# Optimization experiments

Measured on AMD Instinct MI355X. Metric: run time of the kernel, lower is better.

Reference implementation:

```python
import jax, jax.numpy as jnp
import numpy as np

N_NODES = 100000

def gcn_conv(x, W, b, src, dst, n):
    # PyG GCNConv with add_self_loops=True, symmetric normalization.
    # Transform first (reduces feature dim before irregular aggregation).
    h = x @ W  # [N, out]
    # degree with self loops: in-degree over dst plus 1 per node
    deg = jax.ops.segment_sum(jnp.ones_like(dst, dtype=h.dtype), dst, num_segments=n) + 1.0
    dinv = jax.lax.rsqrt(deg)  # deg >= 1 due to self loops
    norm = dinv[src] * dinv[dst]  # [E]
    # message = norm * h[src], aggregated at dst; self-loop term = dinv_i^2 * h_i
    agg = jax.ops.segment_sum(h[src] * norm[:, None], dst, num_segments=n)
    agg = agg + h * (dinv * dinv)[:, None]
    return agg + b

def setup_inputs() -> dict:
    key = jax.random.key(0)
    k1, k2, k3, k4, k5 = jax.random.split(key, 5)
    F_in, H, E_dim = 128, 64, 64
    node_features = jax.random.normal(k1, (N_NODES, F_in), dtype=jnp.float32)
    edge_index = jax.random.randint(k2, (2, 1600000), 0, N_NODES, dtype=jnp.int64)
    s = 1.0 / np.sqrt(F_in)
    W1 = jax.random.uniform(k3, (F_in, H), jnp.float32, -s, s)
    b1 = jnp.zeros((H,), jnp.float32)
    s2 = 1.0 / np.sqrt(H)
    W2 = jax.random.uniform(k4, (H, H), jnp.float32, -s2, s2)
    b2 = jnp.zeros((H,), jnp.float32)
    Wl = jax.random.uniform(k5, (H, E_dim), jnp.float32, -s2, s2)
    bl = jnp.zeros((E_dim,), jnp.float32)
    return {"node_features": node_features, "edge_index": edge_index,
            "W1": W1, "b1": b1, "W2": W2, "b2": b2, "Wl": Wl, "bl": bl}

def reference(node_features, edge_index, W1, b1, W2, b2, Wl, bl):
    src, dst = edge_index[0], edge_index[1]
    n = node_features.shape[0]
    x = node_features.astype(jnp.float32)
    x = jax.nn.relu(gcn_conv(x, W1, b1, src, dst, n))
    # dropout: train=False -> identity
    x = jax.nn.relu(gcn_conv(x, W2, b2, src, dst, n))
    x = x @ Wl + bl
    return jax.nn.sigmoid(x).T  # [embed_size, N]
```

## Files before the change

### kernel.cpp

```cpp
#include <hip/hip_runtime.h>
#include <hip/hip_bf16.h>


#define FEAT 64
#define FIN 128
#define PAD 64
#define CAP 4608
#define EPB 2048
#define MAXNB 512

typedef __attribute__((ext_vector_type(8))) short  short8;
typedef __attribute__((ext_vector_type(4))) float  f32x4;
typedef __attribute__((ext_vector_type(2))) float  float2v;

__device__ __forceinline__ unsigned short f2bf(float f) {
    union { float f; unsigned u; } x; x.f = f;
    unsigned r = x.u + 0x7FFF + ((x.u >> 16) & 1);
    return (unsigned short)(r >> 16);
}
__device__ __forceinline__ float bflo(unsigned u) {
    union { unsigned v; float f; } x; x.v = u << 16; return x.f;
}
__device__ __forceinline__ float bfhi(unsigned u) {
    union { unsigned v; float f; } x; x.v = u & 0xFFFF0000u; return x.f;
}

__global__ void wtrans_kernel(const float* __restrict__ W1, const float* __restrict__ W2,
                              const float* __restrict__ Wl,
                              unsigned short* __restrict__ Wt1, unsigned short* __restrict__ Wt2,
                              unsigned short* __restrict__ Wlt, int* __restrict__ bcnt) {
    int t = blockIdx.x * 256 + threadIdx.x;
    if (t < FIN * 64) {
        int k = t >> 6, n = t & 63;
        Wt1[n * FIN + k] = f2bf(W1[t]);
    } else if (t < FIN * 64 + 64 * 64) {
        int u = t - FIN * 64;
        int k = u >> 6, n = u & 63;
        Wt2[n * 64 + k] = f2bf(W2[u]);
    } else if (t < FIN * 64 + 2 * 64 * 64) {
        int u = t - FIN * 64 - 64 * 64;
        int k = u >> 6, n = u & 63;
        Wlt[n * 64 + k] = f2bf(Wl[u]);
    } else if (t < FIN * 64 + 2 * 64 * 64 + MAXNB * 16) {
        bcnt[t - FIN * 64 - 2 * 64 * 64] = 0;
    }
}

__global__ __launch_bounds__(256) void bin_kernel(const int* __restrict__ ei,
                                                  int* __restrict__ bcnt,
                                                  int* __restrict__ bbuf,
                                                  int E, int nb) {
    __shared__ int hist[MAXNB];
    __shared__ int base[MAXNB];
    for (int t = threadIdx.x; t < nb; t += 256) hist[t] = 0;
    __syncthreads();
    int e0 = blockIdx.x * EPB;
    int sreg[8], dreg[8], preg[8];
#pragma unroll
    for (int k = 0; k < 8; ++k) {
        int idx = e0 + k * 256 + threadIdx.x;
        if (idx < E) {
            sreg[k] = ei[idx];
            dreg[k] = ei[E + idx];
            preg[k] = atomicAdd(&hist[dreg[k] >> 8], 1);
        } else {
            dreg[k] = -1;
        }
    }
    __syncthreads();
    for (int t = threadIdx.x; t < nb; t += 256) {
        int h = hist[t];
        base[t] = (h > 0) ? atomicAdd(&bcnt[t * 16], h) : 0;
    }
    __syncthreads();
#pragma unroll
    for (int k = 0; k < 8; ++k) {
        if (dreg[k] >= 0) {
            int b = dreg[k] >> 8;
            int p = base[b] + preg[k];
            if (p < CAP)
                bbuf[(size_t)b * CAP + p] = sreg[k] | ((dreg[k] & 255) << 20);
        }
    }
}

__global__ __launch_bounds__(256) void ell_from_bins_kernel(const int* __restrict__ bbuf,
                                                            const int* __restrict__ bcnt,
                                                            int* __restrict__ col,
                                                            int* __restrict__ cnt,
                                                            float* __restrict__ dinv,
                                                            unsigned int* __restrict__ gz,
                                                            int N) {
    __shared__ int lcnt[256];
    int b = blockIdx.x;
    int d0 = b << 8;
    lcnt[threadIdx.x] = 0;
    if (b == 0 && threadIdx.x < 32)
        gz[(size_t)N * 32 + threadIdx.x] = 0u;
    __syncthreads();
    int ne = bcnt[b * 16];
    if (ne > CAP) ne = CAP;
    const int* eb = bbuf + (size_t)b * CAP;
    for (int i = threadIdx.x; i < ne; i += 256) {
        int w = eb[i];
        int s = w & 0xFFFFF;
        int dl = w >> 20;
        int slot = atomicAdd(&lcnt[dl], 1);
        if (slot < PAD) col[(size_t)(d0 + dl) * PAD + slot] = s;
    }
    __syncthreads();
    int d = d0 + threadIdx.x;
    if (d < N) {
        int c = lcnt[threadIdx.x];
        if (c > PAD) c = PAD;
        int c8 = (c + 7) & ~7;
        for (int k = c; k < c8; ++k) col[(size_t)d * PAD + k] = N;
        cnt[d] = c;
        dinv[d] = rsqrtf((float)c + 1.0f);
    }
}

__global__ __launch_bounds__(256) void gemm1_mfma_kernel(const float* __restrict__ x,
                                                         const unsigned short* __restrict__ Wt,
                                                         const float* __restrict__ dinv,
                                                         unsigned short* __restrict__ g, int N) {
    const int lane = threadIdx.x & 63;
    const int wave = threadIdx.x >> 6;
    const int m = lane & 15, quad = lane >> 4;
    const int r0 = blockIdx.x * 64 + wave * 16;
    const int arow = r0 + m;
    const bool aok = arow < N;
    f32x4 acc[4] = {f32x4{0,0,0,0}, f32x4{0,0,0,0}, f32x4{0,0,0,0}, f32x4{0,0,0,0}};
    union { short8 s; unsigned short u[8]; } a;
#pragma unroll
    for (int s = 0; s < FIN / 32; ++s) {
        if (aok) {
            const float* xp = x + (size_t)arow * FIN + s * 32 + quad * 8;
            float4 a0 = *(const float4*)xp;
            float4 a1 = *(const float4*)(xp + 4);
            a.u[0] = f2bf(a0.x); a.u[1] = f2bf(a0.y);
            a.u[2] = f2bf(a0.z); a.u[3] = f2bf(a0.w);
            a.u[4] = f2bf(a1.x); a.u[5] = f2bf(a1.y);
            a.u[6] = f2bf(a1.z); a.u[7] = f2bf(a1.w);
        } else {
#pragma unroll
            for (int k = 0; k < 8; ++k) a.u[k] = 0;
        }
#pragma unroll
        for (int t = 0; t < 4; ++t) {
            const unsigned short* bp = Wt + (size_t)(t * 16 + m) * FIN + s * 32 + quad * 8;
            short8 bf = *(const short8*)bp;
            acc[t] = __builtin_amdgcn_mfma_f32_16x16x32_bf16(a.s, bf, acc[t], 0, 0, 0);
        }
    }
    const int rbase = r0 + quad * 4;
#pragma unroll
    for (int i = 0; i < 4; ++i) {
        int r = rbase + i;
        if (r < N) {
            float di = dinv[r];
#pragma unroll
            for (int t = 0; t < 4; ++t)
                g[(size_t)r * 64 + t * 16 + m] = f2bf(di * acc[t][i]);
        }
    }
}

__global__ __launch_bounds__(256) void gemm2_mfma_kernel(const unsigned short* __restrict__ xb,
                                                         const unsigned short* __restrict__ Wt,
                                                         const float* __restrict__ dinv,
                                                         unsigned short* __restrict__ g, int N) {
    const int lane = threadIdx.x & 63;
    const int wave = threadIdx.x >> 6;
    const int m = lane & 15, quad = lane >> 4;
    const int r0 = blockIdx.x * 64 + wave * 16;
    const int arow = r0 + m;
    const bool aok = arow < N;
    f32x4 acc[4] = {f32x4{0,0,0,0}, f32x4{0,0,0,0}, f32x4{0,0,0,0}, f32x4{0,0,0,0}};
    const short8 zero8 = short8{0,0,0,0,0,0,0,0};
#pragma unroll
    for (int s = 0; s < 2; ++s) {
        short8 a = aok ? *(const short8*)(xb + (size_t)arow * 64 + s * 32 + quad * 8) : zero8;
#pragma unroll
        for (int t = 0; t < 4; ++t) {
            short8 bf = *(const short8*)(Wt + (size_t)(t * 16 + m) * 64 + s * 32 + quad * 8);
            acc[t] = __builtin_amdgcn_mfma_f32_16x16x32_bf16(a, bf, acc[t], 0, 0, 0);
        }
    }
    const int rbase = r0 + quad * 4;
#pragma unroll
    for (int i = 0; i < 4; ++i) {
        int r = rbase + i;
        if (r < N) {
            float di = dinv[r];
#pragma unroll
            for (int t = 0; t < 4; ++t)
                g[(size_t)r * 64 + t * 16 + m] = f2bf(di * acc[t][i]);
        }
    }
}

__global__ __launch_bounds__(256) void agg_relu_kernel(const unsigned short* __restrict__ g,
                                                       const int* __restrict__ cnt,
                                                       const int* __restrict__ col,
                                                       const float* __restrict__ dinv,
                                                       const float* __restrict__ b,
                                                       unsigned short* __restrict__ xout, int N) {
    const int lane = threadIdx.x & 63;
    const int wave = threadIdx.x >> 6;
    const int ng = lane >> 3, fc = lane & 7;
    const int node = blockIdx.x * 32 + wave * 8 + ng;
    const bool valid = node < N;
    int c8 = 0;
    if (valid) {
        int c = cnt[node];
        if (c > PAD) c = PAD;
        c8 = (c + 7) & ~7;
    }
    int cmax = c8;
#pragma unroll
    for (int mk = 8; mk <= 32; mk <<= 1) {
        int o = __shfl_xor(cmax, mk, 64);
        cmax = cmax > o ? cmax : o;
    }
    const int* cl = col + (size_t)node * PAD;
    float2v acc0 = {0.f, 0.f}, acc1 = {0.f, 0.f}, acc2 = {0.f, 0.f}, acc3 = {0.f, 0.f};
    {
        uint4 w = *(const uint4*)(g + (size_t)(valid ? node : N) * 64 + fc * 8);
        acc0 += (float2v){bflo(w.x), bfhi(w.x)};
        acc1 += (float2v){bflo(w.y), bfhi(w.y)};
        acc2 += (float2v){bflo(w.z), bfhi(w.z)};
        acc3 += (float2v){bflo(w.w), bfhi(w.w)};
    }
    for (int j = 0; j < cmax; j += 4) {
        bool ok = j < c8;
        int s0 = ok ? cl[j]     : N;
        int s1 = ok ? cl[j + 1] : N;
        int s2 = ok ? cl[j + 2] : N;
        int s3 = ok ? cl[j + 3] : N;
        uint4 w0 = *(const uint4*)(g + (size_t)s0 * 64 + fc * 8);
        uint4 w1 = *(const uint4*)(g + (size_t)s1 * 64 + fc * 8);
        uint4 w2 = *(const uint4*)(g + (size_t)s2 * 64 + fc * 8);
        uint4 w3 = *(const uint4*)(g + (size_t)s3 * 64 + fc * 8);
        acc0 += (float2v){bflo(w0.x), bfhi(w0.x)};
        acc1 += (float2v){bflo(w0.y), bfhi(w0.y)};
        acc2 += (float2v){bflo(w0.z), bfhi(w0.z)};
        acc3 += (float2v){bflo(w0.w), bfhi(w0.w)};
        acc0 += (float2v){bflo(w1.x), bfhi(w1.x)};
        acc1 += (float2v){bflo(w1.y), bfhi(w1.y)};
        acc2 += (float2v){bflo(w1.z), bfhi(w1.z)};
        acc3 += (float2v){bflo(w1.w), bfhi(w1.w)};
        acc0 += (float2v){bflo(w2.x), bfhi(w2.x)};
        acc1 += (float2v){bflo(w2.y), bfhi(w2.y)};
        acc2 += (float2v){bflo(w2.z), bfhi(w2.z)};
        acc3 += (float2v){bflo(w2.w), bfhi(w2.w)};
        acc0 += (float2v){bflo(w3.x), bfhi(w3.x)};
        acc1 += (float2v){bflo(w3.y), bfhi(w3.y)};
        acc2 += (float2v){bflo(w3.z), bfhi(w3.z)};
        acc3 += (float2v){bflo(w3.w), bfhi(w3.w)};
    }
    if (valid) {
        float di = dinv[node];
        float4 b0 = *(const float4*)&b[fc * 8];
        float4 b1 = *(const float4*)&b[fc * 8 + 4];
        union { uint4 v; unsigned short u[8]; } o;
        o.u[0] = f2bf(fmaxf(di * acc0.x + b0.x, 0.f));
        o.u[1] = f2bf(fmaxf(di * acc0.y + b0.y, 0.f));
        o.u[2] = f2bf(fmaxf(di * acc1.x + b0.z, 0.f));
        o.u[3] = f2bf(fmaxf(di * acc1.y + b0.w, 0.f));
        o.u[4] = f2bf(fmaxf(di * acc2.x + b1.x, 0.f));
        o.u[5] = f2bf(fmaxf(di * acc2.y + b1.y, 0.f));
        o.u[6] = f2bf(fmaxf(di * acc3.x + b1.z, 0.f));
        o.u[7] = f2bf(fmaxf(di * acc3.y + b1.w, 0.f));
        *(uint4*)&xout[(size_t)node * 64 + fc * 8] = o.v;
    }
}

__global__ __launch_bounds__(256) void final_mfma_kernel(const unsigned short* __restrict__ x2,
                                                         const unsigned short* __restrict__ Wlt,
                                                         const float* __restrict__ bl,
                                                         float* __restrict__ out, int N) {
    const int lane = threadIdx.x & 63;
    const int wave = threadIdx.x >> 6;
    const int m = lane & 15, quad = lane >> 4;
    const int r0 = blockIdx.x * 64 + wave * 16;
    const int arow = r0 + m;
    const bool aok = arow < N;
    f32x4 acc[4] = {f32x4{0,0,0,0}, f32x4{0,0,0,0}, f32x4{0,0,0,0}, f32x4{0,0,0,0}};
    const short8 zero8 = short8{0,0,0,0,0,0,0,0};
#pragma unroll
    for (int s = 0; s < 2; ++s) {
        short8 a = aok ? *(const short8*)(x2 + (size_t)arow * 64 + s * 32 + quad * 8) : zero8;
#pragma unroll
        for (int t = 0; t < 4; ++t) {
            short8 bf = *(const short8*)(Wlt + (size_t)(t * 16 + m) * 64 + s * 32 + quad * 8);
            acc[t] = __builtin_amdgcn_mfma_f32_16x16x32_bf16(a, bf, acc[t], 0, 0, 0);
        }
    }
    const int rbase = r0 + quad * 4;
    if (rbase + 3 < N && (N & 3) == 0) {
#pragma unroll
        for (int t = 0; t < 4; ++t) {
            int j = t * 16 + m;
            float bj = bl[j];
            float4 o;
            o.x = 1.f / (1.f + __expf(-(acc[t][0] + bj)));
            o.y = 1.f / (1.f + __expf(-(acc[t][1] + bj)));
            o.z = 1.f / (1.f + __expf(-(acc[t][2] + bj)));
            o.w = 1.f / (1.f + __expf(-(acc[t][3] + bj)));
            *(float4*)&out[(size_t)j * N + rbase] = o;
        }
    } else {
#pragma unroll
        for (int t = 0; t < 4; ++t) {
            int j = t * 16 + m;
            float bj = bl[j];
#pragma unroll
            for (int i = 0; i < 4; ++i) {
                int r = rbase + i;
                if (r < N)
                    out[(size_t)j * N + r] = 1.f / (1.f + __expf(-(acc[t][i] + bj)));
            }
        }
    }
}

extern "C" void kernel_launch(void* const* d_in, const int* in_sizes, int n_in,
                              void* d_out, int out_size, void* d_ws, size_t ws_size,
                              hipStream_t stream) {
    const float* x   = (const float*)d_in[0];
    const int*   ei  = (const int*)d_in[1];
    const float* W1  = (const float*)d_in[2];
    const float* b1  = (const float*)d_in[3];
    const float* W2  = (const float*)d_in[4];
    const float* b2  = (const float*)d_in[5];
    const float* Wl  = (const float*)d_in[6];
    const float* bl  = (const float*)d_in[7];
    float*       out = (float*)d_out;

    int N  = in_sizes[0] / FIN;
    int E  = in_sizes[1] / 2;
    int nb = (N + 255) >> 8;
    int ng = (N + 63) >> 6;

    int*            bcnt = (int*)d_ws;
    unsigned short* Wt1  = (unsigned short*)(bcnt + MAXNB * 16);
    unsigned short* Wt2  = Wt1 + FIN * 64;
    unsigned short* Wlt  = Wt2 + 64 * 64;
    int*            cnt  = (int*)(Wlt + 64 * 64);
    float*          dinv = (float*)(cnt + N);
    int*            col  = (int*)(dinv + N);
    int*            bbuf = col + (size_t)N * PAD;
    unsigned short* bufG = (unsigned short*)bbuf;
    unsigned short* bufX = bufG + (size_t)(N + 1) * FEAT;

    int wtot = FIN * 64 + 2 * 64 * 64 + MAXNB * 16;
    wtrans_kernel<<<(wtot + 255) / 256, 256, 0, stream>>>(W1, W2, Wl, Wt1, Wt2, Wlt, bcnt);

    bin_kernel<<<(E + EPB - 1) / EPB, 256, 0, stream>>>(ei, bcnt, bbuf, E, nb);
    ell_from_bins_kernel<<<nb, 256, 0, stream>>>(bbuf, bcnt, col, cnt, dinv,
                                                 (unsigned int*)bufG, N);

    gemm1_mfma_kernel<<<ng, 256, 0, stream>>>(x, Wt1, dinv, bufG, N);
    agg_relu_kernel<<<(N + 31) / 32, 256, 0, stream>>>(bufG, cnt, col, dinv, b1, bufX, N);

    gemm2_mfma_kernel<<<ng, 256, 0, stream>>>(bufX, Wt2, dinv, bufG, N);
    agg_relu_kernel<<<(N + 31) / 32, 256, 0, stream>>>(bufG, cnt, col, dinv, b2, bufX, N);

    final_mfma_kernel<<<ng, 256, 0, stream>>>(bufX, Wlt, bl, out, N);
}
```

Measured before the change: 268.1 us.

## Replace atomic bin reservation with histogram, column scan, and deterministic scatter

Edge binning switches from one kernel that reserves global bin offsets with atomics into padded counters to three passes. A per-block histogram pass is followed by a per-bin exclusive scan across blocks, then a scatter pass that re-reads the edges and writes them at the precomputed offsets. This removes global atomic contention and makes bin placement block-ordered. In exchange it adds two launches, re-reads the edge index, and moves per-block histograms through global memory.

Result: faster. 257.1 us (-4.1%).

```diff
diff --git a/kernel.cpp b/kernel.cpp
--- a/kernel.cpp
+++ b/kernel.cpp
@@ -6,8 +6,9 @@
 #define FIN 128
 #define PAD 64
 #define CAP 4608
-#define EPB 2048
+#define EPB2 4096
 #define MAXNB 512
+#define NBP 512
 
 typedef __attribute__((ext_vector_type(8))) short  short8;
 typedef __attribute__((ext_vector_type(4))) float  f32x4;
@@ -28,7 +29,7 @@
 __global__ void wtrans_kernel(const float* __restrict__ W1, const float* __restrict__ W2,
                               const float* __restrict__ Wl,
                               unsigned short* __restrict__ Wt1, unsigned short* __restrict__ Wt2,
-                              unsigned short* __restrict__ Wlt, int* __restrict__ bcnt) {
+                              unsigned short* __restrict__ Wlt) {
     int t = blockIdx.x * 256 + threadIdx.x;
     if (t < FIN * 64) {
         int k = t >> 6, n = t & 63;
@@ -41,45 +42,71 @@
         int u = t - FIN * 64 - 64 * 64;
         int k = u >> 6, n = u & 63;
         Wlt[n * 64 + k] = f2bf(Wl[u]);
-    } else if (t < FIN * 64 + 2 * 64 * 64 + MAXNB * 16) {
-        bcnt[t - FIN * 64 - 2 * 64 * 64] = 0;
-    }
-}
-
-__global__ __launch_bounds__(256) void bin_kernel(const int* __restrict__ ei,
-                                                  int* __restrict__ bcnt,
-                                                  int* __restrict__ bbuf,
-                                                  int E, int nb) {
+    }
+}
+
+__global__ __launch_bounds__(256) void hist_kernel(const int* __restrict__ ei,
+                                                   int* __restrict__ hist2,
+                                                   int E, int nb) {
+    __shared__ int hist[MAXNB];
+    for (int t = threadIdx.x; t < nb; t += 256) hist[t] = 0;
+    __syncthreads();
+    int e0 = blockIdx.x * EPB2;
+#pragma unroll
+    for (int k = 0; k < EPB2 / 256; ++k) {
+        int idx = e0 + k * 256 + threadIdx.x;
+        if (idx < E) atomicAdd(&hist[ei[E + idx] >> 8], 1);
+    }
+    __syncthreads();
+    for (int t = threadIdx.x; t < nb; t += 256)
+        hist2[(size_t)blockIdx.x * NBP + t] = hist[t];
+}
+
+__global__ __launch_bounds__(256) void scan_kernel(int* __restrict__ hist2,
+                                                   int* __restrict__ bcnt,
+                                                   int nblk) {
+    __shared__ int v[512];
+    const int t = threadIdx.x;
+    const int b = blockIdx.x;
+    v[t]       = (t < nblk)       ? hist2[(size_t)t * NBP + b]         : 0;
+    v[t + 256] = (t + 256 < nblk) ? hist2[(size_t)(t + 256) * NBP + b] : 0;
+    __syncthreads();
+#pragma unroll
+    for (int off = 1; off < 512; off <<= 1) {
+        int x0 = (t >= off) ? v[t - off] : 0;
+        int x1 = v[t + 256 - off];
+        __syncthreads();
+        v[t] += x0; v[t + 256] += x1;
+        __syncthreads();
+    }
+    if (t < nblk)       hist2[(size_t)t * NBP + b]         = (t == 0) ? 0 : v[t - 1];
+    if (t + 256 < nblk) hist2[(size_t)(t + 256) * NBP + b] = v[t + 255];
+    if (t == 0) bcnt[b] = v[nblk - 1];
+}
+
+__global__ __launch_bounds__(256) void scatter_kernel(const int* __restrict__ ei,
+                                                      const int* __restrict__ hist2,
+                                                      int* __restrict__ bbuf,
+                                                      int E, int nb) {
     __shared__ int hist[MAXNB];
     __shared__ int base[MAXNB];
-    for (int t = threadIdx.x; t < nb; t += 256) hist[t] = 0;
-    __syncthreads();
-    int e0 = blockIdx.x * EPB;
-    int sreg[8], dreg[8], preg[8];
-#pragma unroll
-    for (int k = 0; k < 8; ++k) {
+    for (int t = threadIdx.x; t < nb; t += 256) {
+        hist[t] = 0;
+        base[t] = hist2[(size_t)blockIdx.x * NBP + t];
+    }
+    __syncthreads();
+    int e0 = blockIdx.x * EPB2;
+#pragma unroll
+    for (int k = 0; k < EPB2 / 256; ++k) {
         int idx = e0 + k * 256 + threadIdx.x;
         if (idx < E) {
-            sreg[k] = ei[idx];
-            dreg[k] = ei[E + idx];
-            preg[k] = atomicAdd(&hist[dreg[k] >> 8], 1);
-        } else {
-            dreg[k] = -1;
-        }
-    }
-    __syncthreads();
-    for (int t = threadIdx.x; t < nb; t += 256) {
-        int h = hist[t];
-        base[t] = (h > 0) ? atomicAdd(&bcnt[t * 16], h) : 0;
-    }
-    __syncthreads();
-#pragma unroll
-    for (int k = 0; k < 8; ++k) {
-        if (dreg[k] >= 0) {
-            int b = dreg[k] >> 8;
-            int p = base[b] + preg[k];
+            int s = ei[idx];
+            int d = ei[E + idx];
+            int b = d >> 8;
+            int r = atomicAdd(&hist[b], 1);
+            int p = base[b] + r;
             if (p < CAP)
-                bbuf[(size_t)b * CAP + p] = sreg[k] | ((dreg[k] & 255) << 20);
+                bbuf[(size_t)b * CAP + p] = s | ((d & 255) << 20);
         }
     }
 }
@@ -98,7 +125,7 @@
     if (b == 0 && threadIdx.x < 32)
         gz[(size_t)N * 32 + threadIdx.x] = 0u;
     __syncthreads();
-    int ne = bcnt[b * 16];
+    int ne = bcnt[b];
     if (ne > CAP) ne = CAP;
     const int* eb = bbuf + (size_t)b * CAP;
     for (int i = threadIdx.x; i < ne; i += 256) {
@@ -338,26 +365,30 @@
     const float* bl  = (const float*)d_in[7];
     float*       out = (float*)d_out;
 
-    int N  = in_sizes[0] / FIN;
-    int E  = in_sizes[1] / 2;
-    int nb = (N + 255) >> 8;
-    int ng = (N + 63) >> 6;
-
-    int*            bcnt = (int*)d_ws;
-    unsigned short* Wt1  = (unsigned short*)(bcnt + MAXNB * 16);
-    unsigned short* Wt2  = Wt1 + FIN * 64;
-    unsigned short* Wlt  = Wt2 + 64 * 64;
-    int*            cnt  = (int*)(Wlt + 64 * 64);
-    float*          dinv = (float*)(cnt + N);
-    int*            col  = (int*)(dinv + N);
-    int*            bbuf = col + (size_t)N * PAD;
-    unsigned short* bufG = (unsigned short*)bbuf;
-    unsigned short* bufX = bufG + (size_t)(N + 1) * FEAT;
-
-    int wtot = FIN * 64 + 2 * 64 * 64 + MAXNB * 16;
-    wtrans_kernel<<<(wtot + 255) / 256, 256, 0, stream>>>(W1, W2, Wl, Wt1, Wt2, Wlt, bcnt);
-
-    bin_kernel<<<(E + EPB - 1) / EPB, 256, 0, stream>>>(ei, bcnt, bbuf, E, nb);
+    int N    = in_sizes[0] / FIN;
+    int E    = in_sizes[1] / 2;
+    int nb   = (N + 255) >> 8;
+    int nblk = (E + EPB2 - 1) / EPB2;
+    int ng   = (N + 63) >> 6;
+
+    int*            bcnt  = (int*)d_ws;
+    int*            hist2 = bcnt + 512;
+    unsigned short* Wt1   = (unsigned short*)(hist2 + 512 * NBP);
+    unsigned short* Wt2   = Wt1 + FIN * 64;
+    unsigned short* Wlt   = Wt2 + 64 * 64;
+    int*            cnt   = (int*)(Wlt + 64 * 64);
+    float*          dinv  = (float*)(cnt + N);
+    int*            col   = (int*)(dinv + N);
+    int*            bbuf  = col + (size_t)N * PAD;
+    unsigned short* bufG  = (unsigned short*)bbuf;
+    unsigned short* bufX  = bufG + (size_t)(N + 1) * FEAT;
+
+    int wtot = FIN * 64 + 2 * 64 * 64;
+    wtrans_kernel<<<(wtot + 255) / 256, 256, 0, stream>>>(W1, W2, Wl, Wt1, Wt2, Wlt);
+
+    hist_kernel<<<nblk, 256, 0, stream>>>(ei, hist2, E, nb);
+    scan_kernel<<<nb, 256, 0, stream>>>(hist2, bcnt, nblk);
+    scatter_kernel<<<nblk, 256, 0, stream>>>(ei, hist2, bbuf, E, nb);
     ell_from_bins_kernel<<<nb, 256, 0, stream>>>(bbuf, bcnt, col, cnt, dinv,
                                                  (unsigned int*)bufG, N);
 
```
